# Kernel optimization log

Measured on AMD Instinct MI355X. Metric: run time of the kernel, lower is better.

## Reference

```python
import jax, jax.numpy as jnp
import numpy as np

# Config (matches init_kwargs)
B, H, N, K, M = 64, 2, 512, 64, 16  # batch, num_of_hom, max_num_of_points, K, man_dim
EPS = 1e-7
MAX_NORM = 1.0 - 1e-5  # clip radius strictly inside the Poincare ball


def _norm(x):
    return jnp.sqrt(jnp.sum(x * x, axis=-1, keepdims=True))


def _exp0(v):
    # Poincare exp map at origin (c=1): tanh(||v||) * v / ||v||
    n = jnp.maximum(_norm(v), EPS)
    return jnp.tanh(n) * v / n


def _log0(y):
    # Poincare log map at origin (c=1): arctanh(||y||) * y / ||y||, norm clipped inside ball
    n = jnp.maximum(_norm(y), EPS)
    return jnp.arctanh(jnp.minimum(n, MAX_NORM)) * y / n


def _process_dgm(dgm, theta_h):
    # dgm: (B, N, 2)  theta_h: (K, M)
    b = dgm.shape[0]
    td = jnp.tile(dgm, (1, K, 1))                        # (B, K*N, 2) -- K blocks of N points
    td = jnp.pad(td, ((0, 0), (0, 0), (0, M - 2)))       # (B, K*N, M)
    tt = jnp.tile(theta_h, (1, N)).reshape(-1, M)        # (K*N, M) -- theta_k repeated N times
    x = _exp0(td) + tt                                   # parametrization + learned offset
    tangent_x = _log0(x)                                 # log map to tangent space at origin
    tangent_x = tangent_x.reshape(b, N, K, M)            # mirrors TF reshape exactly (row-major)
    sums = jnp.sum(tangent_x, axis=1)                    # (B, K, M)
    x_dgm = _exp0(sums)                                  # exp map back to manifold
    y_dgm = _log0(x_dgm)                                 # chart coordinates
    return y_dgm.reshape(-1, K, M)


def setup_inputs() -> dict:
    key = jax.random.key(0)
    k1, k2 = jax.random.split(key)
    inputs = jax.random.uniform(k1, (B, H, N, 2), dtype=jnp.float32)   # (birth, death) pairs
    theta = jax.random.uniform(k2, (H, K, M), dtype=jnp.float32) * 0.05  # tf.random_uniform_initializer
    return {"inputs": inputs, "theta": theta}


def reference(inputs, theta):
    out_0 = _process_dgm(inputs[:, 0, :, :], theta[0])[:, None, :, :]  # (B,1,K,M)
    out_1 = _process_dgm(inputs[:, 1, :, :], theta[1])[:, None, :, :]  # (B,1,K,M)
    return jnp.concatenate([out_0, out_1], axis=1)                      # (B,2,K,M)
```

## Files before the change

### kernel.cpp

```cpp
#include <hip/hip_runtime.h>

constexpr int Bsz = 64;
constexpr int Hn  = 2;
constexpr int Np  = 512;
constexpr int Kk  = 64;
constexpr int Mm  = 16;

#define EPSf      1e-7f
#define MAXN      (1.0f - 1e-5f)
#define ATANH_MAX 6.1030338f

__global__ __launch_bounds__(256) void PManifold_kernel(
    const float* __restrict__ inp,
    const float* __restrict__ theta,
    float* __restrict__ out)
{
    const int tid  = threadIdx.x;
    const int lane = tid & 63;
    const int wav  = tid >> 6;
    const int g    = blockIdx.x * 4 + wav;
    const int kp   = g & 63;
    const int bh   = g >> 6;
    const int h    = bh & (Hn - 1);

    const float4* tq = reinterpret_cast<const float4*>(theta) + (size_t)(h * Kk + lane) * 4;
    float t[16];
    {
        float4 q0 = tq[0], q1 = tq[1], q2 = tq[2], q3 = tq[3];
        t[0]=q0.x; t[1]=q0.y; t[2]=q0.z; t[3]=q0.w;
        t[4]=q1.x; t[5]=q1.y; t[6]=q1.z; t[7]=q1.w;
        t[8]=q2.x; t[9]=q2.y; t[10]=q2.z; t[11]=q2.w;
        t[12]=q3.x; t[13]=q3.y; t[14]=q3.z; t[15]=q3.w;
    }

    float c = 0.0f;
    #pragma unroll
    for (int m = 2; m < 16; ++m) c = fmaf(t[m], t[m], c);

    const float2* ip = reinterpret_cast<const float2*>(inp) + (size_t)bh * Np + kp;
    float e0[8], e1[8];
    #pragma unroll
    for (int p = 0; p < 8; ++p) {
        float2 dd = ip[p << 6];
        float d0 = dd.x, d1 = dd.y;
        float nd = sqrtf(fmaf(d0, d0, d1 * d1));
        float nc = fmaxf(nd, EPSf);
        float ex = __expf(2.0f * nc);
        float th = 1.0f - __fdividef(2.0f, ex + 1.0f);
        float sc = __fdividef(th, nc);
        e0[p] = sc * d0;
        e1[p] = sc * d1;
    }

    const float t0 = t[0], t1 = t[1];
    float A = 0.0f, S0 = 0.0f, S1 = 0.0f;
    #pragma unroll
    for (int p = 0; p < 8; ++p) {
        float x0 = e0[p] + t0;
        float x1 = e1[p] + t1;
        float r  = sqrtf(fmaf(x0, x0, fmaf(x1, x1, c)));
        float rn = fmaxf(r, EPSf);
        float rc = fminf(rn, MAXN);
        float at = 0.5f * __logf(__fdividef(1.0f + rc, 1.0f - rc));
        float a  = __fdividef(at, rn);
        A += a;
        S0 = fmaf(a, x0, S0);
        S1 = fmaf(a, x1, S1);
    }

    float v[16];
    v[0] = S0;
    v[1] = S1;
    #pragma unroll
    for (int m = 2; m < 16; ++m) v[m] = A * t[m];

    #pragma unroll
    for (int off = 32; off > 0; off >>= 1) {
        #pragma unroll
        for (int m = 0; m < 16; ++m) v[m] += __shfl_xor(v[m], off, 64);
    }

    float nn2 = 0.0f;
    #pragma unroll
    for (int m = 0; m < 16; ++m) nn2 = fmaf(v[m], v[m], nn2);
    float nn  = fmaxf(sqrtf(nn2), EPSf);
    float gsc = (nn < ATANH_MAX) ? 1.0f : __fdividef(ATANH_MAX, nn);

    if (lane == 0) {
        float4* op = reinterpret_cast<float4*>(out + (size_t)g * Mm);
        op[0] = make_float4(gsc*v[0],  gsc*v[1],  gsc*v[2],  gsc*v[3]);
        op[1] = make_float4(gsc*v[4],  gsc*v[5],  gsc*v[6],  gsc*v[7]);
        op[2] = make_float4(gsc*v[8],  gsc*v[9],  gsc*v[10], gsc*v[11]);
        op[3] = make_float4(gsc*v[12], gsc*v[13], gsc*v[14], gsc*v[15]);
    }
}

extern "C" void kernel_launch(void* const* d_in, const int* in_sizes, int n_in,
                              void* d_out, int out_size, void* d_ws, size_t ws_size,
                              hipStream_t stream) {
    const float* inp   = (const float*)d_in[0];
    const float* theta = (const float*)d_in[1];
    float*       out   = (float*)d_out;

    const int total_waves = Bsz * Hn * Kk;
    dim3 grid(total_waves / 4), block(256);
    hipLaunchKernelGGL(PManifold_kernel, grid, block, 0, stream, inp, theta, out);
}
```

Before: 68.70 us.

## Replace 16-wide shuffle reduction with LDS matvec and readlane input sharing

Each wave now loads one input point per lane and broadcasts the eight exp-mapped points with readlane, instead of every lane loading all eight. The final reduction over K becomes a small matrix-vector product through shared memory (S0, S1 and A weighted by theta), rather than 16 separate shuffle-reduction chains. Log and arctanh use rsqrt and log2 with a folded constant. This cuts shuffle traffic and per-lane work but adds two __syncthreads and LDS accesses.

```diff
diff --git a/kernel.cpp b/kernel.cpp
--- a/kernel.cpp
+++ b/kernel.cpp
@@ -9,12 +9,16 @@
 #define EPSf      1e-7f
 #define MAXN      (1.0f - 1e-5f)
 #define ATANH_MAX 6.1030338f
+#define HALF_LN2  0.34657359f
 
 __global__ __launch_bounds__(256) void PManifold_kernel(
     const float* __restrict__ inp,
     const float* __restrict__ theta,
     float* __restrict__ out)
 {
+    __shared__ float sTheta[Kk * 17];
+    __shared__ float sRed[4][196];
+
     const int tid  = threadIdx.x;
     const int lane = tid & 63;
     const int wav  = tid >> 6;
@@ -23,75 +27,94 @@
     const int bh   = g >> 6;
     const int h    = bh & (Hn - 1);
 
-    const float4* tq = reinterpret_cast<const float4*>(theta) + (size_t)(h * Kk + lane) * 4;
-    float t[16];
     {
+        const int r  = tid >> 2;
+        const int cb = (tid & 3) << 2;
+        const float4 q = *reinterpret_cast<const float4*>(theta + (size_t)(h * Kk + r) * Mm + cb);
+        sTheta[r * 17 + cb + 0] = q.x;
+        sTheta[r * 17 + cb + 1] = q.y;
+        sTheta[r * 17 + cb + 2] = q.z;
+        sTheta[r * 17 + cb + 3] = q.w;
+    }
+    __syncthreads();
+
+    float t0, t1, c;
+    {
+        const float4* tq = reinterpret_cast<const float4*>(theta) + (size_t)(h * Kk + lane) * 4;
         float4 q0 = tq[0], q1 = tq[1], q2 = tq[2], q3 = tq[3];
-        t[0]=q0.x; t[1]=q0.y; t[2]=q0.z; t[3]=q0.w;
-        t[4]=q1.x; t[5]=q1.y; t[6]=q1.z; t[7]=q1.w;
-        t[8]=q2.x; t[9]=q2.y; t[10]=q2.z; t[11]=q2.w;
-        t[12]=q3.x; t[13]=q3.y; t[14]=q3.z; t[15]=q3.w;
+        t0 = q0.x; t1 = q0.y;
+        c  = q0.z * q0.z + q0.w * q0.w;
+        c  = fmaf(q1.x, q1.x, fmaf(q1.y, q1.y, fmaf(q1.z, q1.z, fmaf(q1.w, q1.w, c))));
+        c  = fmaf(q2.x, q2.x, fmaf(q2.y, q2.y, fmaf(q2.z, q2.z, fmaf(q2.w, q2.w, c))));
+        c  = fmaf(q3.x, q3.x, fmaf(q3.y, q3.y, fmaf(q3.z, q3.z, fmaf(q3.w, q3.w, c))));
     }
 
-    float c = 0.0f;
-    #pragma unroll
-    for (int m = 2; m < 16; ++m) c = fmaf(t[m], t[m], c);
-
-    const float2* ip = reinterpret_cast<const float2*>(inp) + (size_t)bh * Np + kp;
-    float e0[8], e1[8];
-    #pragma unroll
-    for (int p = 0; p < 8; ++p) {
-        float2 dd = ip[p << 6];
-        float d0 = dd.x, d1 = dd.y;
-        float nd = sqrtf(fmaf(d0, d0, d1 * d1));
+    float E0, E1;
+    {
+        const int p = lane & 7;
+        const float2* ip = reinterpret_cast<const float2*>(inp) + (size_t)bh * Np;
+        float2 dd = ip[(p << 6) + kp];
+        float nd = sqrtf(fmaf(dd.x, dd.x, dd.y * dd.y));
         float nc = fmaxf(nd, EPSf);
         float ex = __expf(2.0f * nc);
         float th = 1.0f - __fdividef(2.0f, ex + 1.0f);
         float sc = __fdividef(th, nc);
-        e0[p] = sc * d0;
-        e1[p] = sc * d1;
+        E0 = sc * dd.x;
+        E1 = sc * dd.y;
+    }
+    float e0[8], e1[8];
+    #pragma unroll
+    for (int p = 0; p < 8; ++p) {
+        e0[p] = __int_as_float(__builtin_amdgcn_readlane(__float_as_int(E0), p));
+        e1[p] = __int_as_float(__builtin_amdgcn_readlane(__float_as_int(E1), p));
     }
 
-    const float t0 = t[0], t1 = t[1];
-    float A = 0.0f, S0 = 0.0f, S1 = 0.0f;
+    float At = 0.0f, S0 = 0.0f, S1 = 0.0f;
     #pragma unroll
     for (int p = 0; p < 8; ++p) {
         float x0 = e0[p] + t0;
         float x1 = e1[p] + t1;
-        float r  = sqrtf(fmaf(x0, x0, fmaf(x1, x1, c)));
-        float rn = fmaxf(r, EPSf);
-        float rc = fminf(rn, MAXN);
-        float at = 0.5f * __logf(__fdividef(1.0f + rc, 1.0f - rc));
-        float a  = __fdividef(at, rn);
-        A += a;
+        float u  = fmaf(x0, x0, fmaf(x1, x1, c));
+        u        = fmaxf(u, 1e-14f);
+        float rs = rsqrtf(u);
+        float rc = fminf(u * rs, MAXN);
+        float Q  = (1.0f + rc) * __fdividef(1.0f, 1.0f - rc);
+        float tt = __log2f(Q) * rs;
+        float a  = HALF_LN2 * tt;
+        At += tt;
         S0 = fmaf(a, x0, S0);
         S1 = fmaf(a, x1, S1);
     }
+    const float A = HALF_LN2 * At;
 
-    float v[16];
-    v[0] = S0;
-    v[1] = S1;
+    sRed[wav][lane]       = S0;
+    sRed[wav][65 + lane]  = S1;
+    sRed[wav][130 + lane] = A;
+    __syncthreads();
+
+    const int m = lane & 15;
+    const int q = lane >> 4;
+    const int base = (m == 0) ? 0 : ((m == 1) ? 65 : 130);
+    float acc = 0.0f;
     #pragma unroll
-    for (int m = 2; m < 16; ++m) v[m] = A * t[m];
+    for (int j = 0; j < 16; ++j) {
+        int   k   = (q << 4) + j;
+        float val = sRed[wav][base + k];
+        float mu  = sTheta[k * 17 + m];
+        mu = (m < 2) ? 1.0f : mu;
+        acc = fmaf(val, mu, acc);
+    }
+    acc += __shfl_xor(acc, 16, 64);
+    acc += __shfl_xor(acc, 32, 64);
 
+    float w = acc * acc;
     #pragma unroll
-    for (int off = 32; off > 0; off >>= 1) {
-        #pragma unroll
-        for (int m = 0; m < 16; ++m) v[m] += __shfl_xor(v[m], off, 64);
-    }
-
-    float nn2 = 0.0f;
-    #pragma unroll
-    for (int m = 0; m < 16; ++m) nn2 = fmaf(v[m], v[m], nn2);
-    float nn  = fmaxf(sqrtf(nn2), EPSf);
+    for (int off = 1; off < 16; off <<= 1) w += __shfl_xor(w, off, 64);
+    float nn  = fmaxf(sqrtf(w), EPSf);
     float gsc = (nn < ATANH_MAX) ? 1.0f : __fdividef(ATANH_MAX, nn);
 
-    if (lane == 0) {
-        float4* op = reinterpret_cast<float4*>(out + (size_t)g * Mm);
-        op[0] = make_float4(gsc*v[0],  gsc*v[1],  gsc*v[2],  gsc*v[3]);
-        op[1] = make_float4(gsc*v[4],  gsc*v[5],  gsc*v[6],  gsc*v[7]);
-        op[2] = make_float4(gsc*v[8],  gsc*v[9],  gsc*v[10], gsc*v[11]);
-        op[3] = make_float4(gsc*v[12], gsc*v[13], gsc*v[14], gsc*v[15]);
+    if (lane < 16) {
+        out[(size_t)g * Mm + m] = gsc * acc;
     }
 }
 
```

Result: faster. 60.77 us (-11.5%).
